# Optimization experiments

Measured on AMD Instinct MI355X. Metric: run time of the kernel, lower is better.

Reference implementation:

```python
import jax, jax.numpy as jnp
import numpy as np

B, S, D = 2, 2048, 2048
H, HKV = 16, 4
GROUPS = H // HKV
RQ, RKV = 1024, 512
DH, DR = 192, 64          # q_head_dim, rope dim
DN = DH - DR              # nrope dim = 128
DV = 128                  # v head dim
EPS = 1e-20


def setup_inputs() -> dict:
    key = jax.random.key(0)
    ks = jax.random.split(key, 8)
    inp = {
        "hidden_states": jax.random.normal(ks[0], (B, S, D), jnp.float32),
        # causal mask (0 = masked), as used by masked_fill(mask == 0, -inf)
        "attention_mask": jnp.tril(jnp.ones((S, S), jnp.int32))[None, None],
        "w_qa": jax.random.normal(ks[1], (D, RQ), jnp.float32) * 0.02,
        "b_qa": jnp.zeros((RQ,), jnp.float32),
        "g_q": jnp.ones((RQ,), jnp.float32),
        "w_qb": jax.random.normal(ks[2], (RQ, H * DH), jnp.float32) * 0.02,
        "b_qb": jnp.zeros((H * DH,), jnp.float32),
        "w_kva": jax.random.normal(ks[3], (D, RKV + DR), jnp.float32) * 0.02,
        "b_kva": jnp.zeros((RKV + DR,), jnp.float32),
        "g_kv": jnp.ones((RKV,), jnp.float32),
        "w_kvb": jax.random.normal(ks[4], (RKV, HKV * (DN + DV)), jnp.float32) * 0.02,
        "b_kvb": jnp.zeros((HKV * (DN + DV),), jnp.float32),
        "w_o": jax.random.normal(ks[5], (H * DV, D), jnp.float32) * 0.02,
        "b_o": jnp.zeros((D,), jnp.float32),
    }
    return inp


def _rmsnorm(x, g, eps=EPS):
    var = jnp.mean(x * x, axis=-1, keepdims=True)
    return x * jax.lax.rsqrt(var + eps) * g


def _rope_cos_sin(seq_len, dim, base=10000.0, dtype=jnp.float32):
    inv_freq = 1.0 / (base ** (jnp.arange(0, dim, 2, dtype=jnp.float32) / dim))
    t = jnp.arange(seq_len, dtype=jnp.float32)
    freqs = jnp.outer(t, inv_freq)                    # [S, dim/2]
    emb = jnp.concatenate([freqs, freqs], axis=-1)    # [S, dim]
    return jnp.cos(emb).astype(dtype), jnp.sin(emb).astype(dtype)


def _apply_rope(x, cos, sin):
    # x: [..., S, dr]; rotate_half convention
    d2 = x.shape[-1] // 2
    x1, x2 = x[..., :d2], x[..., d2:]
    rot = jnp.concatenate([-x2, x1], axis=-1)
    return x * cos + rot * sin


def reference(hidden_states, attention_mask, w_qa, b_qa, g_q, w_qb, b_qb,
              w_kva, b_kva, g_kv, w_kvb, b_kvb, w_o, b_o):
    b, s, _ = hidden_states.shape
    # --- Q: LoRA down -> RMSNorm -> LoRA up ---
    q_a = hidden_states @ w_qa + b_qa                         # [B,S,RQ]
    q_b = _rmsnorm(q_a, g_q) @ w_qb + b_qb                    # [B,S,H*DH]
    q_b = q_b.reshape(b, s, H, DH).transpose(0, 2, 1, 3)      # [B,H,S,DH]
    q_nrope, q_rope = q_b[..., :DN], q_b[..., DN:]
    # --- KV: LoRA down, split latent / shared rope key ---
    kv_a = hidden_states @ w_kva + b_kva                      # [B,S,RKV+DR]
    kv_c, k_rope = kv_a[..., :RKV], kv_a[..., RKV:]
    kv_b = _rmsnorm(kv_c, g_kv) @ w_kvb + b_kvb               # [B,S,HKV*(DN+DV)]
    kv_b = kv_b.reshape(b, s, HKV, DN + DV).transpose(0, 2, 1, 3)
    k_nrope, value_states = kv_b[..., :DN], kv_b[..., DN:]    # [B,HKV,S,DN/DV]
    # --- split RoPE ---
    cos, sin = _rope_cos_sin(s, DR, dtype=hidden_states.dtype)
    q_rope = _apply_rope(q_rope, cos, sin)                    # [B,H,S,DR]
    k_rope = _apply_rope(k_rope[:, None], cos, sin)           # [B,1,S,DR]
    # --- assemble heads (rope part first, matching source concat order) ---
    query_states = jnp.concatenate([q_rope, q_nrope], axis=-1)            # [B,H,S,DH]
    key_states = jnp.concatenate(
        [jnp.broadcast_to(k_rope, (b, HKV, s, DR)), k_nrope], axis=-1)    # [B,HKV,S,DH]
    # --- GQA expand kv heads ---
    key_states = jnp.repeat(key_states, GROUPS, axis=1)                   # [B,H,S,DH]
    value_states = jnp.repeat(value_states, GROUPS, axis=1)               # [B,H,S,DV]
    # --- attention ---
    scores = jnp.einsum('bhqd,bhkd->bhqk', query_states, key_states)
    scores = scores / jnp.sqrt(jnp.asarray(DH, scores.dtype))
    scores = jnp.where(attention_mask == 0, jnp.asarray(-1e9, scores.dtype), scores)
    weights = jax.nn.softmax(scores, axis=-1)
    attn_out = jnp.einsum('bhqk,bhkd->bhqd', weights, value_states)       # [B,H,S,DV]
    attn_out = attn_out.transpose(0, 2, 1, 3).reshape(b, s, H * DV)
    return attn_out @ w_o + b_o
```

## Files before the change

kernel.cpp:

```cpp
#include <hip/hip_runtime.h>
#include <hip/hip_bf16.h>
#include <stdint.h>

#define DEV static __device__ __forceinline__

typedef __attribute__((ext_vector_type(8))) short bf16x8;
typedef __attribute__((ext_vector_type(4))) float f32x4;
typedef __attribute__((ext_vector_type(16))) float f32x16;

constexpr int Bc = 2, Sc = 2048, Dc = 2048;
constexpr int Hc = 16, HKVc = 4;
constexpr int RQc = 1024, RKVc = 512;
constexpr int DHc = 192, DRc = 64, DVc = 128;

DEV unsigned short f2bf(float f) {
  union { float f; uint32_t u; } v; v.f = f;
  uint32_t r = v.u + 0x7FFFu + ((v.u >> 16) & 1u);
  return (unsigned short)(r >> 16);
}
DEV float bf2f(unsigned short u) {
  union { uint32_t u; float f; } v; v.u = ((uint32_t)u) << 16;
  return v.f;
}

DEV void gload_lds16(const unsigned short* g, unsigned short* l) {
  __builtin_amdgcn_global_load_lds(
      (const __attribute__((address_space(1))) unsigned int*)g,
      (__attribute__((address_space(3))) unsigned int*)l, 16, 0, 0);
}

__global__ void f2b_kernel(const float* __restrict__ in, unsigned short* __restrict__ out, int n) {
  int stride = gridDim.x * blockDim.x;
  for (int i = blockIdx.x * blockDim.x + threadIdx.x; i * 4 < n; i += stride) {
    float4 v = reinterpret_cast<const float4*>(in)[i];
    union { unsigned short u[4]; uint64_t q; } pk;
    pk.u[0] = f2bf(v.x); pk.u[1] = f2bf(v.y); pk.u[2] = f2bf(v.z); pk.u[3] = f2bf(v.w);
    reinterpret_cast<uint64_t*>(out)[i] = pk.q;
  }
}

__global__ void wtrans_kernel(const float* __restrict__ in, unsigned short* __restrict__ out,
                              int R, int C) {
  __shared__ float tile[32][33];
  const int c0 = blockIdx.x * 32, r0 = blockIdx.y * 32;
  const int tx = threadIdx.x & 31, ty = threadIdx.x >> 5;
#pragma unroll
  for (int i = 0; i < 32; i += 8)
    tile[ty + i][tx] = in[(size_t)(r0 + ty + i) * C + c0 + tx];
  __syncthreads();
#pragma unroll
  for (int i = 0; i < 32; i += 8)
    out[(size_t)(c0 + ty + i) * R + r0 + tx] = f2bf(tile[tx][ty + i]);
}

__global__ void rope_table_kernel(float* __restrict__ cosT, float* __restrict__ sinT) {
  int idx = blockIdx.x * blockDim.x + threadIdx.x;
  if (idx >= Sc * DRc) return;
  int t = idx >> 6;
  int j = idx & 63;
  float inv = exp2f(-13.287712379549449f * (float)(j & 31) * (1.0f / 32.0f));
  float f = (float)t * inv;
  cosT[idx] = cosf(f);
  sinT[idx] = sinf(f);
}

template<int R>
__global__ void rmsnorm_kernel(const float* __restrict__ in, int istride,
                               const float* __restrict__ g, unsigned short* __restrict__ out) {
  int row = blockIdx.x;
  const float* x = in + (size_t)row * istride;
  float ss = 0.f;
  for (int j = threadIdx.x; j < R; j += 256) { float v = x[j]; ss += v * v; }
  for (int off = 32; off; off >>= 1) ss += __shfl_down(ss, off, 64);
  __shared__ float wsum[4];
  if ((threadIdx.x & 63) == 0) wsum[threadIdx.x >> 6] = ss;
  __syncthreads();
  float tot = wsum[0] + wsum[1] + wsum[2] + wsum[3];
  float rs = rsqrtf(tot * (1.0f / R) + 1e-20f);
  for (int j = threadIdx.x; j < R; j += 256)
    out[(size_t)row * R + j] = f2bf(x[j] * rs * g[j]);
}

template<bool OUT_BF16, bool NG>
__global__ __launch_bounds__(256)
void gemm_tn_kernel(const unsigned short* __restrict__ A, const unsigned short* __restrict__ Bt,
                    const float* __restrict__ bias, void* __restrict__ Cout,
                    int M, int N, int K) {
  __shared__ __align__(16) unsigned short As[2][128 * 64];
  __shared__ __align__(16) unsigned short Bs[2][128 * 64];
  const int t = threadIdx.x, lane = t & 63, wave = t >> 6;
  const int wm = wave >> 1, wn = wave & 1;
  const int m0 = blockIdx.x * 128, n0 = blockIdx.y * 128;
  const int fr = lane & 15, fo = (lane >> 4) * 8, rg = lane >> 4;
  const int srow = lane >> 3;
  const int scol = (lane & 7) * 8;

  const unsigned short* Ap[4];
  const unsigned short* Bp[4];
#pragma unroll
  for (int i = 0; i < 4; ++i) {
    const int ar = m0 + wave * 32 + i * 8 + srow;
    Ap[i] = A + (size_t)ar * K + scol;
    int br = n0 + wave * 32 + i * 8 + srow;
    if (NG) br = br < N ? br : N - 1;
    Bp[i] = Bt + (size_t)br * K + scol;
  }

  auto stage = [&](int buf, int k0) {
#pragma unroll
    for (int i = 0; i < 4; ++i) {
      gload_lds16(Ap[i] + k0, &As[buf][(wave * 32 + i * 8) * 64]);
      gload_lds16(Bp[i] + k0, &Bs[buf][(wave * 32 + i * 8) * 64]);
    }
  };

  f32x4 acc[4][4] = {};
  const int nt = K >> 6;

  stage(0, 0);
  for (int tt = 0; tt < nt; ++tt) {
    const int cur = tt & 1;
    if (tt + 1 < nt) {
      stage(cur ^ 1, (tt + 1) * 64);
      asm volatile("s_waitcnt vmcnt(8)" ::: "memory");
    } else {
      asm volatile("s_waitcnt vmcnt(0)" ::: "memory");
    }
    __syncthreads();
#pragma unroll
    for (int kk = 0; kk < 64; kk += 32) {
      bf16x8 af[4], bf[4];
#pragma unroll
      for (int m = 0; m < 4; ++m)
        af[m] = *reinterpret_cast<const bf16x8*>(&As[cur][(wm * 64 + m * 16 + fr) * 64 + kk + fo]);
#pragma unroll
      for (int n = 0; n < 4; ++n)
        bf[n] = *reinterpret_cast<const bf16x8*>(&Bs[cur][(wn * 64 + n * 16 + fr) * 64 + kk + fo]);
      __builtin_amdgcn_s_setprio(1);
#pragma unroll
      for (int m = 0; m < 4; ++m)
#pragma unroll
        for (int n = 0; n < 4; ++n)
          acc[m][n] = __builtin_amdgcn_mfma_f32_16x16x32_bf16(af[m], bf[n], acc[m][n], 0, 0, 0);
      __builtin_amdgcn_s_setprio(0);
    }
    __syncthreads();
  }

#pragma unroll
  for (int m = 0; m < 4; ++m) {
    const int row = m0 + wm * 64 + m * 16 + rg * 4;
#pragma unroll
    for (int n = 0; n < 4; ++n) {
      const int col = n0 + wn * 64 + n * 16 + fr;
      if (NG && col >= N) continue;
      const float bb = bias[col];
#pragma unroll
      for (int r = 0; r < 4; ++r) {
        float v = acc[m][n][r] + bb;
        if (OUT_BF16)
          reinterpret_cast<unsigned short*>(Cout)[(size_t)(row + r) * N + col] = f2bf(v);
        else
          reinterpret_cast<float*>(Cout)[(size_t)(row + r) * N + col] = v;
      }
    }
  }
}

__global__ void prep_q_kernel(const unsigned short* __restrict__ qb,
                              const float* __restrict__ cosT, const float* __restrict__ sinT,
                              unsigned short* __restrict__ Q) {
  const float QS = 0.07216878364870323f * 1.4426950408889634f;
  int bs = blockIdx.x;
  int s = bs & (Sc - 1);
  int b = bs >> 11;
  int d = threadIdx.x;
  if (d >= 192) return;
  for (int h = 0; h < Hc; ++h) {
    const unsigned short* src = qb + (size_t)bs * (Hc * DHc) + h * DHc;
    float v;
    if (d < 128) {
      v = bf2f(src[d]);
    } else {
      int j = d - 128;
      float x = bf2f(src[128 + j]);
      float other = bf2f(src[128 + (j < 32 ? j + 32 : j - 32)]);
      float c = cosT[s * 64 + j], sn = sinT[s * 64 + j];
      v = (j < 32) ? (x * c - other * sn) : (x * c + other * sn);
    }
    Q[(((size_t)(b * Hc + h)) * Sc + s) * DHc + d] = f2bf(v * QS);
  }
}

__global__ void prep_k_kernel(const unsigned short* __restrict__ kvb,
                              const float* __restrict__ ccat,
                              const float* __restrict__ cosT, const float* __restrict__ sinT,
                              unsigned short* __restrict__ K) {
  int bs = blockIdx.x;
  int s = bs & (Sc - 1);
  int b = bs >> 11;
  int d = threadIdx.x;
  if (d >= 192) return;
  unsigned short ropeval = 0;
  if (d >= 128) {
    int j = d - 128;
    float x = ccat[(size_t)bs * 1600 + 1536 + j];
    float other = ccat[(size_t)bs * 1600 + 1536 + (j < 32 ? j + 32 : j - 32)];
    float c = cosT[s * 64 + j], sn = sinT[s * 64 + j];
    float v = (j < 32) ? (x * c - other * sn) : (x * c + other * sn);
    ropeval = f2bf(v);
  }
  const size_t off = (size_t)(s >> 5) * 6144 + (d >> 3) * 256 + (s & 31) * 8 + (d & 7);
  for (int kvh = 0; kvh < HKVc; ++kvh) {
    unsigned short o;
    if (d < 128) o = kvb[(size_t)bs * 1024 + kvh * 256 + d];
    else o = ropeval;
    K[(size_t)(b * HKVc + kvh) * Sc * DHc + off] = o;
  }
}

__global__ void vtrans_kernel(const unsigned short* __restrict__ kvb, unsigned short* __restrict__ Vt) {
  int idx = blockIdx.x;
  int dt = idx & 3;  idx >>= 2;
  int st = idx & 63; idx >>= 6;
  int kvh = idx & 3; idx >>= 2;
  int b = idx;
  __shared__ unsigned short tile[32][33];
  int t = threadIdx.x;
  int c = t & 31, r0 = t >> 5;
#pragma unroll
  for (int i = 0; i < 4; ++i) {
    int r = r0 + i * 8;
    int s = st * 32 + r;
    tile[r][c] = kvb[((size_t)(b * Sc + s)) * 1024 + kvh * 256 + 128 + dt * 32 + c];
  }
  __syncthreads();
#pragma unroll
  for (int i = 0; i < 4; ++i) {
    int r = r0 + i * 8;
    const int dd = dt * 32 + r;
    const int k = st * 32 + c;
    const size_t pos = (size_t)(k >> 5) * 4096 + ((k >> 3) & 3) * 1024 + dd * 8 + (k & 7);
    Vt[(size_t)((b * HKVc + kvh)) * DVc * Sc + pos] = tile[c][r];
  }
}

__global__ __launch_bounds__(256)
void attn_kernel(const unsigned short* __restrict__ Q, const unsigned short* __restrict__ Kt,
                 const unsigned short* __restrict__ Vt, unsigned short* __restrict__ attnOut) {
  __shared__ __align__(16) unsigned short Ks[4][6144];
  __shared__ float mlS[4][2][32];

  const int bid = blockIdx.x;
  const int g = bid & 7;
  const int b = g >> 2, kvh = g & 3;
  const int rr = bid >> 3;
  const int hp = rr & 1;
  const int u = rr >> 1;
  const int w = threadIdx.x >> 6;
  const int hd = w >> 1;
  const int sp = w & 1;
  const int h = kvh * 4 + hp * 2 + hd;
  const int lane = threadIdx.x & 63;
  const int l31 = lane & 31, hi = lane >> 5;

  const unsigned short* Qh = Q + (size_t)(b * Hc + h) * Sc * DHc;
  const unsigned short* Kg = Kt + (size_t)(b * HKVc + kvh) * Sc * DHc;
  const unsigned short* Vg = Vt + (size_t)(b * HKVc + kvh) * DVc * Sc;

  auto stage = [&](int i) {
    const unsigned short* src = Kg + (size_t)i * 12288;
    unsigned short* dst = &Ks[(i & 1) * 2][0];
#pragma unroll
    for (int j = 0; j < 6; ++j)
      gload_lds16(src + j * 2048 + threadIdx.x * 8, dst + j * 2048 + threadIdx.x * 8);
  };

#pragma unroll 1
  for (int pan = 0; pan < 2; ++pan) {
    const int sub = pan ? u : (63 - u);
    const int q0 = sub * 32;
    const int q = q0 + l31;
    const int NS = (sub >> 1) + 1;

    bf16x8 qf[12];
#pragma unroll
    for (int f = 0; f < 12; ++f)
      qf[f] = *reinterpret_cast<const bf16x8*>(Qh + (size_t)q * DHc + f * 16 + hi * 8);

    f32x16 ot[4] = {};
    float m = -INFINITY, lsum = 0.f;

    stage(0);
    asm volatile("s_waitcnt vmcnt(0)" ::: "memory");
    __syncthreads();

    for (int i = 0; i < NS; ++i) {
      const int t = 2 * i + sp;
      const bool active = (t <= sub);
      const int p = i & 1;

      bf16x8 vf[8];
      if (active) {
#pragma unroll
        for (int dt = 0; dt < 4; ++dt)
#pragma unroll
          for (int k2 = 0; k2 < 2; ++k2)
            vf[dt * 2 + k2] = *reinterpret_cast<const bf16x8*>(
                Vg + (size_t)t * 4096 + (k2 * 2 + hi) * 1024 + (dt * 32 + l31) * 8);
      }
      __builtin_amdgcn_sched_barrier(0);
      if (i + 1 < NS) stage(i + 1);
      __builtin_amdgcn_sched_barrier(0);

      if (active) {
        const unsigned short* kb = &Ks[p * 2 + sp][0];
        f32x16 s = {};
        __builtin_amdgcn_s_setprio(1);
#pragma unroll
        for (int f = 0; f < 12; ++f) {
          bf16x8 kf = *reinterpret_cast<const bf16x8*>(kb + (f * 2 + hi) * 256 + l31 * 8);
          s = __builtin_amdgcn_mfma_f32_32x32x16_bf16(kf, qf[f], s, 0, 0, 0);
        }
        __builtin_amdgcn_s_setprio(0);

        float v[16];
        if (t == sub) {
#pragma unroll
          for (int rrr = 0; rrr < 16; ++rrr) {
            const int kl = (rrr & 3) + 8 * (rrr >> 2) + 4 * hi;
            v[rrr] = (kl <= l31) ? s[rrr] : -3.0e38f;
          }
        } else {
#pragma unroll
          for (int rrr = 0; rrr < 16; ++rrr) v[rrr] = s[rrr];
        }

        float pmax = fmaxf(fmaxf(fmaxf(v[0], v[1]), fmaxf(v[2], v[3])),
                           fmaxf(fmaxf(v[4], v[5]), fmaxf(v[6], v[7])));
        float pmax2 = fmaxf(fmaxf(fmaxf(v[8], v[9]), fmaxf(v[10], v[11])),
                            fmaxf(fmaxf(v[12], v[13]), fmaxf(v[14], v[15])));
        pmax = fmaxf(pmax, pmax2);
        pmax = fmaxf(pmax, __shfl_xor(pmax, 32, 64));

        float cf = 1.f;
        if (!__all(pmax - m <= 8.0f)) {
          const float mnew = fmaxf(m, pmax);
          cf = exp2f(m - mnew);
          m = mnew;
#pragma unroll
          for (int dt = 0; dt < 4; ++dt)
#pragma unroll
            for (int rrr = 0; rrr < 16; ++rrr) ot[dt][rrr] *= cf;
        }

        float pp[16];
        float rs = 0.f;
#pragma unroll
        for (int rrr = 0; rrr < 16; ++rrr) { pp[rrr] = exp2f(v[rrr] - m); rs += pp[rrr]; }
        rs += __shfl_xor(rs, 32, 64);
        lsum = lsum * cf + rs;

        uint32_t c[8], x[8];
#pragma unroll
        for (int ii = 0; ii < 8; ++ii) {
          asm("v_cvt_pk_bf16_f32 %0, %1, %2" : "=v"(c[ii]) : "v"(pp[2 * ii]), "v"(pp[2 * ii + 1]));
          x[ii] = (uint32_t)__shfl_xor((int)c[ii], 32, 64);
        }
        union { uint32_t w[4]; bf16x8 v8; } pa0, pa1;
        pa0.w[0] = hi ? x[2] : c[0];
        pa0.w[1] = hi ? x[3] : c[1];
        pa0.w[2] = hi ? c[2] : x[0];
        pa0.w[3] = hi ? c[3] : x[1];
        pa1.w[0] = hi ? x[6] : c[4];
        pa1.w[1] = hi ? x[7] : c[5];
        pa1.w[2] = hi ? c[6] : x[4];
        pa1.w[3] = hi ? c[7] : x[5];

        __builtin_amdgcn_s_setprio(1);
#pragma unroll
        for (int dt = 0; dt < 4; ++dt) {
          ot[dt] = __builtin_amdgcn_mfma_f32_32x32x16_bf16(vf[dt * 2], pa0.v8, ot[dt], 0, 0, 0);
          ot[dt] = __builtin_amdgcn_mfma_f32_32x32x16_bf16(vf[dt * 2 + 1], pa1.v8, ot[dt], 0, 0, 0);
        }
        __builtin_amdgcn_s_setprio(0);
      }

      asm volatile("s_waitcnt vmcnt(0)" ::: "memory");
      __syncthreads();
    }

    if (hi == 0) { mlS[w][0][l31] = m; mlS[w][1][l31] = lsum; }
    __syncthreads();
    const int pw = w ^ 1;
    const float mp = mlS[pw][0][l31];
    const float lp = mlS[pw][1][l31];
    const float mstar = fmaxf(m, mp);
    const float sc = exp2f(m - mstar);
    const float lstar = lsum * sc + lp * exp2f(mp - mstar);
    float* LO = (float*)&Ks[0][0];

    if (sp == 1) {
#pragma unroll
      for (int dt = 0; dt < 4; ++dt)
#pragma unroll
        for (int rq = 0; rq < 4; ++rq) {
          float4 vv;
          vv.x = ot[dt][rq * 4 + 0] * sc;
          vv.y = ot[dt][rq * 4 + 1] * sc;
          vv.z = ot[dt][rq * 4 + 2] * sc;
          vv.w = ot[dt][rq * 4 + 3] * sc;
          *reinterpret_cast<float4*>(&LO[(size_t)(hd * 32 + l31) * 132 + dt * 32 + 8 * rq + 4 * hi]) = vv;
        }
    }
    __syncthreads();
    if (sp == 0) {
      const float inv = 1.0f / lstar;
      unsigned short* dst = attnOut + ((size_t)(b * Sc + q)) * (Hc * DVc) + h * DVc;
#pragma unroll
      for (int dt = 0; dt < 4; ++dt)
#pragma unroll
        for (int rq = 0; rq < 4; ++rq) {
          float4 pv = *reinterpret_cast<const float4*>(
              &LO[(size_t)(hd * 32 + l31) * 132 + dt * 32 + 8 * rq + 4 * hi]);
          const float o0 = (ot[dt][rq * 4 + 0] * sc + pv.x) * inv;
          const float o1 = (ot[dt][rq * 4 + 1] * sc + pv.y) * inv;
          const float o2 = (ot[dt][rq * 4 + 2] * sc + pv.z) * inv;
          const float o3 = (ot[dt][rq * 4 + 3] * sc + pv.w) * inv;
          uint2 pk;
          pk.x = (uint32_t)f2bf(o0) | ((uint32_t)f2bf(o1) << 16);
          pk.y = (uint32_t)f2bf(o2) | ((uint32_t)f2bf(o3) << 16);
          *reinterpret_cast<uint2*>(dst + dt * 32 + 8 * rq + 4 * hi) = pk;
        }
    }
    __syncthreads();
  }
}

extern "C" void kernel_launch(void* const* d_in, const int* in_sizes, int n_in,
                              void* d_out, int out_size, void* d_ws, size_t ws_size,
                              hipStream_t stream) {
  (void)in_sizes; (void)n_in; (void)out_size; (void)ws_size;
  const float* hidden = (const float*)d_in[0];
  const float* w_qa  = (const float*)d_in[2];
  const float* b_qa  = (const float*)d_in[3];
  const float* g_q   = (const float*)d_in[4];
  const float* w_qb  = (const float*)d_in[5];
  const float* b_qb  = (const float*)d_in[6];
  const float* w_kva = (const float*)d_in[7];
  const float* b_kva = (const float*)d_in[8];
  const float* g_kv  = (const float*)d_in[9];
  const float* w_kvb = (const float*)d_in[10];
  const float* b_kvb = (const float*)d_in[11];
  const float* w_o   = (const float*)d_in[12];
  const float* b_o   = (const float*)d_in[13];
  float* out = (float*)d_out;

  char* ws = (char*)d_ws;
  size_t off = 0;
  auto alloc = [&](size_t bytes) -> void* {
    void* p = ws + off;
    off += (bytes + 255) & ~(size_t)255;
    return p;
  };
  const int MS = Bc * Sc;
  const int NCAT = RQc + RKVc + DRc;

  unsigned short* Xbf   = (unsigned short*)alloc((size_t)MS * Dc * 2);
  unsigned short* Wcat  = (unsigned short*)alloc((size_t)NCAT * Dc * 2);
  unsigned short* WqbT  = (unsigned short*)alloc((size_t)Hc * DHc * RQc * 2);
  unsigned short* WkvbT = (unsigned short*)alloc((size_t)HKVc * 256 * RKVc * 2);
  unsigned short* WoT   = (unsigned short*)alloc((size_t)Dc * Hc * DVc * 2);
  float* bcat = (float*)alloc((size_t)NCAT * 4);
  float* cosT = (float*)alloc((size_t)Sc * DRc * 4);
  float* sinT = (float*)alloc((size_t)Sc * DRc * 4);
  float* Ccat = (float*)alloc((size_t)MS * NCAT * 4);
  unsigned short* qan  = (unsigned short*)alloc((size_t)MS * RQc * 2);
  unsigned short* qb   = (unsigned short*)alloc((size_t)MS * Hc * DHc * 2);
  unsigned short* kvcn = (unsigned short*)alloc((size_t)MS * RKVc * 2);
  unsigned short* kvb  = (unsigned short*)alloc((size_t)MS * HKVc * 256 * 2);
  unsigned short* Qt   = (unsigned short*)alloc((size_t)Bc * Hc * Sc * DHc * 2);
  unsigned short* Kt   = (unsigned short*)alloc((size_t)Bc * HKVc * Sc * DHc * 2);
  unsigned short* Vt   = (unsigned short*)alloc((size_t)Bc * HKVc * DVc * Sc * 2);
  unsigned short* attnb= (unsigned short*)alloc((size_t)MS * Hc * DVc * 2);

  f2b_kernel<<<dim3(512), dim3(256), 0, stream>>>(hidden, Xbf, MS * Dc);
  wtrans_kernel<<<dim3(RQc / 32, Dc / 32), 256, 0, stream>>>(w_qa, Wcat, Dc, RQc);
  wtrans_kernel<<<dim3((RKVc + DRc) / 32, Dc / 32), 256, 0, stream>>>(w_kva, Wcat + (size_t)RQc * Dc, Dc, RKVc + DRc);
  wtrans_kernel<<<dim3(Hc * DHc / 32, RQc / 32), 256, 0, stream>>>(w_qb, WqbT, RQc, Hc * DHc);
  wtrans_kernel<<<dim3(HKVc * 256 / 32, RKVc / 32), 256, 0, stream>>>(w_kvb, WkvbT, RKVc, HKVc * 256);
  wtrans_kernel<<<dim3(Dc / 32, Hc * DVc / 32), 256, 0, stream>>>(w_o, WoT, Hc * DVc, Dc);
  hipMemcpyAsync(bcat, b_qa, (size_t)RQc * 4, hipMemcpyDeviceToDevice, stream);
  hipMemcpyAsync(bcat + RQc, b_kva, (size_t)(RKVc + DRc) * 4, hipMemcpyDeviceToDevice, stream);
  rope_table_kernel<<<dim3(512), dim3(256), 0, stream>>>(cosT, sinT);

  gemm_tn_kernel<false, true><<<dim3(MS / 128, (NCAT + 127) / 128), 256, 0, stream>>>(Xbf, Wcat, bcat, Ccat, MS, NCAT, Dc);
  rmsnorm_kernel<1024><<<dim3(MS), 256, 0, stream>>>(Ccat, NCAT, g_q, qan);
  rmsnorm_kernel<512><<<dim3(MS), 256, 0, stream>>>(Ccat + RQc, NCAT, g_kv, kvcn);
  gemm_tn_kernel<true, false><<<dim3(MS / 128, Hc * DHc / 128), 256, 0, stream>>>(qan, WqbT, b_qb, qb, MS, Hc * DHc, RQc);
  gemm_tn_kernel<true, false><<<dim3(MS / 128, HKVc * 256 / 128), 256, 0, stream>>>(kvcn, WkvbT, b_kvb, kvb, MS, HKVc * 256, RKVc);

  prep_q_kernel<<<dim3(MS), 256, 0, stream>>>(qb, cosT, sinT, Qt);
  prep_k_kernel<<<dim3(MS), 256, 0, stream>>>(kvb, Ccat, cosT, sinT, Kt);
  vtrans_kernel<<<dim3(Bc * HKVc * (Sc / 32) * (DVc / 32)), 256, 0, stream>>>(kvb, Vt);

  attn_kernel<<<dim3(512), dim3(256), 0, stream>>>(Qt, Kt, Vt, attnb);

  gemm_tn_kernel<false, false><<<dim3(MS / 128, Dc / 128), 256, 0, stream>>>(attnb, WoT, b_o, out, MS, Dc, Hc * DVc);
}
```

Measured before the change: 365.1 us.

## Fuse Q rope/scale/transpose into q-up GEMM; drop attention key-split across waves

```diff
diff --git a/kernel.cpp b/kernel.cpp
--- a/kernel.cpp
+++ b/kernel.cpp
@@ -167,28 +167,99 @@
   }
 }
 
-__global__ void prep_q_kernel(const unsigned short* __restrict__ qb,
-                              const float* __restrict__ cosT, const float* __restrict__ sinT,
-                              unsigned short* __restrict__ Q) {
+__global__ __launch_bounds__(256)
+void gemm_qfuse_kernel(const unsigned short* __restrict__ A, const unsigned short* __restrict__ Bt,
+                       const float* __restrict__ bias,
+                       const float* __restrict__ cosT, const float* __restrict__ sinT,
+                       unsigned short* __restrict__ Qt, int M, int N, int K) {
   const float QS = 0.07216878364870323f * 1.4426950408889634f;
-  int bs = blockIdx.x;
-  int s = bs & (Sc - 1);
-  int b = bs >> 11;
-  int d = threadIdx.x;
-  if (d >= 192) return;
-  for (int h = 0; h < Hc; ++h) {
-    const unsigned short* src = qb + (size_t)bs * (Hc * DHc) + h * DHc;
-    float v;
-    if (d < 128) {
-      v = bf2f(src[d]);
+  __shared__ __align__(16) unsigned short As[2][128 * 64];
+  __shared__ __align__(16) unsigned short Bs[2][128 * 64];
+  const int t = threadIdx.x, lane = t & 63, wave = t >> 6;
+  const int wm = wave >> 1, wn = wave & 1;
+  const int m0 = blockIdx.x * 128, n0 = blockIdx.y * 128;
+  const int fr = lane & 15, fo = (lane >> 4) * 8, rg = lane >> 4;
+  const int srow = lane >> 3;
+  const int scol = (lane & 7) * 8;
+
+  const unsigned short* Ap[4];
+  const unsigned short* Bp[4];
+#pragma unroll
+  for (int i = 0; i < 4; ++i) {
+    Ap[i] = A + (size_t)(m0 + wave * 32 + i * 8 + srow) * K + scol;
+    Bp[i] = Bt + (size_t)(n0 + wave * 32 + i * 8 + srow) * K + scol;
+  }
+
+  auto stage = [&](int buf, int k0) {
+#pragma unroll
+    for (int i = 0; i < 4; ++i) {
+      gload_lds16(Ap[i] + k0, &As[buf][(wave * 32 + i * 8) * 64]);
+      gload_lds16(Bp[i] + k0, &Bs[buf][(wave * 32 + i * 8) * 64]);
+    }
+  };
+
+  f32x4 acc[4][4] = {};
+  const int nt = K >> 6;
+
+  stage(0, 0);
+  for (int tt = 0; tt < nt; ++tt) {
+    const int cur = tt & 1;
+    if (tt + 1 < nt) {
+      stage(cur ^ 1, (tt + 1) * 64);
+      asm volatile("s_waitcnt vmcnt(8)" ::: "memory");
     } else {
-      int j = d - 128;
-      float x = bf2f(src[128 + j]);
-      float other = bf2f(src[128 + (j < 32 ? j + 32 : j - 32)]);
-      float c = cosT[s * 64 + j], sn = sinT[s * 64 + j];
-      v = (j < 32) ? (x * c - other * sn) : (x * c + other * sn);
-    }
-    Q[(((size_t)(b * Hc + h)) * Sc + s) * DHc + d] = f2bf(v * QS);
+      asm volatile("s_waitcnt vmcnt(0)" ::: "memory");
+    }
+    __syncthreads();
+#pragma unroll
+    for (int kk = 0; kk < 64; kk += 32) {
+      bf16x8 af[4], bf[4];
+#pragma unroll
+      for (int m = 0; m < 4; ++m)
+        af[m] = *reinterpret_cast<const bf16x8*>(&As[cur][(wm * 64 + m * 16 + fr) * 64 + kk + fo]);
+#pragma unroll
+      for (int n = 0; n < 4; ++n)
+        bf[n] = *reinterpret_cast<const bf16x8*>(&Bs[cur][(wn * 64 + n * 16 + fr) * 64 + kk + fo]);
+      __builtin_amdgcn_s_setprio(1);
+#pragma unroll
+      for (int m = 0; m < 4; ++m)
+#pragma unroll
+        for (int n = 0; n < 4; ++n)
+          acc[m][n] = __builtin_amdgcn_mfma_f32_16x16x32_bf16(af[m], bf[n], acc[m][n], 0, 0, 0);
+      __builtin_amdgcn_s_setprio(0);
+    }
+    __syncthreads();
+  }
+
+  const int wbase = n0 + wn * 64;
+  const int hq = wbase / 192;
+  const int dbase = wbase - hq * 192;
+  const bool ropewin = (dbase == 128);
+
+#pragma unroll
+  for (int m = 0; m < 4; ++m) {
+    const int row0 = m0 + wm * 64 + m * 16 + rg * 4;
+#pragma unroll
+    for (int n = 0; n < 4; ++n) {
+      const int col = wbase + n * 16 + fr;
+      const int d = dbase + n * 16 + fr;
+      const float bb = bias[col];
+#pragma unroll
+      for (int r = 0; r < 4; ++r) {
+        const int row = row0 + r;
+        const int s = row & (Sc - 1);
+        const int bq = row >> 11;
+        float qv = acc[m][n][r] + bb;
+        if (ropewin) {
+          const int j = d - 128;
+          const int n2 = (n < 2) ? n + 2 : n - 2;
+          const float pv = acc[m][n2][r] + bias[wbase + n2 * 16 + fr];
+          const float c = cosT[s * 64 + j], sn = sinT[s * 64 + j];
+          qv = (n < 2) ? (qv * c - pv * sn) : (qv * c + pv * sn);
+        }
+        Qt[((size_t)(bq * Hc + hq) * Sc + s) * DHc + d] = f2bf(qv * QS);
+      }
+    }
   }
 }
 
@@ -245,11 +316,10 @@
   }
 }
 
-__global__ __launch_bounds__(256)
+__global__ __launch_bounds__(128)
 void attn_kernel(const unsigned short* __restrict__ Q, const unsigned short* __restrict__ Kt,
                  const unsigned short* __restrict__ Vt, unsigned short* __restrict__ attnOut) {
-  __shared__ __align__(16) unsigned short Ks[4][6144];
-  __shared__ float mlS[4][2][32];
+  __shared__ __align__(16) unsigned short Ks[2][2][6144];
 
   const int bid = blockIdx.x;
   const int g = bid & 7;
@@ -258,9 +328,7 @@
   const int hp = rr & 1;
   const int u = rr >> 1;
   const int w = threadIdx.x >> 6;
-  const int hd = w >> 1;
-  const int sp = w & 1;
-  const int h = kvh * 4 + hp * 2 + hd;
+  const int h = kvh * 4 + hp * 2 + w;
   const int lane = threadIdx.x & 63;
   const int l31 = lane & 31, hi = lane >> 5;
 
@@ -268,12 +336,12 @@
   const unsigned short* Kg = Kt + (size_t)(b * HKVc + kvh) * Sc * DHc;
   const unsigned short* Vg = Vt + (size_t)(b * HKVc + kvh) * DVc * Sc;
 
-  auto stage = [&](int i) {
-    const unsigned short* src = Kg + (size_t)i * 12288;
-    unsigned short* dst = &Ks[(i & 1) * 2][0];
-#pragma unroll
-    for (int j = 0; j < 6; ++j)
-      gload_lds16(src + j * 2048 + threadIdx.x * 8, dst + j * 2048 + threadIdx.x * 8);
+  auto stage = [&](int t) {
+    const unsigned short* src = Kg + (size_t)t * 6144;
+    unsigned short* dst = &Ks[w][t & 1][0];
+#pragma unroll
+    for (int j = 0; j < 12; ++j)
+      gload_lds16(src + j * 512 + lane * 8, dst + j * 512 + lane * 8);
   };
 
 #pragma unroll 1
@@ -281,7 +349,7 @@
     const int sub = pan ? u : (63 - u);
     const int q0 = sub * 32;
     const int q = q0 + l31;
-    const int NS = (sub >> 1) + 1;
+    const int NT = sub + 1;
 
     bf16x8 qf[12];
 #pragma unroll
@@ -292,148 +360,109 @@
     float m = -INFINITY, lsum = 0.f;
 
     stage(0);
-    asm volatile("s_waitcnt vmcnt(0)" ::: "memory");
-    __syncthreads();
-
-    for (int i = 0; i < NS; ++i) {
-      const int t = 2 * i + sp;
-      const bool active = (t <= sub);
-      const int p = i & 1;
-
+
+    for (int t = 0; t < NT; ++t) {
       bf16x8 vf[8];
-      if (active) {
+#pragma unroll
+      for (int dt = 0; dt < 4; ++dt)
+#pragma unroll
+        for (int k2 = 0; k2 < 2; ++k2)
+          vf[dt * 2 + k2] = *reinterpret_cast<const bf16x8*>(
+              Vg + (size_t)t * 4096 + (k2 * 2 + hi) * 1024 + (dt * 32 + l31) * 8);
+      __builtin_amdgcn_sched_barrier(0);
+      if (t + 1 < NT) {
+        stage(t + 1);
+        asm volatile("s_waitcnt vmcnt(20)" ::: "memory");
+      } else {
+        asm volatile("s_waitcnt vmcnt(8)" ::: "memory");
+      }
+      __builtin_amdgcn_sched_barrier(0);
+
+      const unsigned short* kb = &Ks[w][t & 1][0];
+      f32x16 s = {};
+      __builtin_amdgcn_s_setprio(1);
+#pragma unroll
+      for (int f = 0; f < 12; ++f) {
+        bf16x8 kf = *reinterpret_cast<const bf16x8*>(kb + (f * 2 + hi) * 256 + l31 * 8);
+        s = __builtin_amdgcn_mfma_f32_32x32x16_bf16(kf, qf[f], s, 0, 0, 0);
+      }
+      __builtin_amdgcn_s_setprio(0);
+
+      float v[16];
+      if (t == sub) {
+#pragma unroll
+        for (int rrr = 0; rrr < 16; ++rrr) {
+          const int kl = (rrr & 3) + 8 * (rrr >> 2) + 4 * hi;
+          v[rrr] = (kl <= l31) ? s[rrr] : -3.0e38f;
+        }
+      } else {
+#pragma unroll
+        for (int rrr = 0; rrr < 16; ++rrr) v[rrr] = s[rrr];
+      }
+
+      float pmax = fmaxf(fmaxf(fmaxf(v[0], v[1]), fmaxf(v[2], v[3])),
+                         fmaxf(fmaxf(v[4], v[5]), fmaxf(v[6], v[7])));
+      float pmax2 = fmaxf(fmaxf(fmaxf(v[8], v[9]), fmaxf(v[10], v[11])),
+                          fmaxf(fmaxf(v[12], v[13]), fmaxf(v[14], v[15])));
+      pmax = fmaxf(pmax, pmax2);
+      pmax = fmaxf(pmax, __shfl_xor(pmax, 32, 64));
+
+      float cf = 1.f;
+      if (!__all(pmax - m <= 8.0f)) {
+        const float mnew = fmaxf(m, pmax);
+        cf = exp2f(m - mnew);
+        m = mnew;
 #pragma unroll
         for (int dt = 0; dt < 4; ++dt)
 #pragma unroll
-          for (int k2 = 0; k2 < 2; ++k2)
-            vf[dt * 2 + k2] = *reinterpret_cast<const bf16x8*>(
-                Vg + (size_t)t * 4096 + (k2 * 2 + hi) * 1024 + (dt * 32 + l31) * 8);
-      }
-      __builtin_amdgcn_sched_barrier(0);
-      if (i + 1 < NS) stage(i + 1);
-      __builtin_amdgcn_sched_barrier(0);
-
-      if (active) {
-        const unsigned short* kb = &Ks[p * 2 + sp][0];
-        f32x16 s = {};
-        __builtin_amdgcn_s_setprio(1);
-#pragma unroll
-        for (int f = 0; f < 12; ++f) {
-          bf16x8 kf = *reinterpret_cast<const bf16x8*>(kb + (f * 2 + hi) * 256 + l31 * 8);
-          s = __builtin_amdgcn_mfma_f32_32x32x16_bf16(kf, qf[f], s, 0, 0, 0);
-        }
-        __builtin_amdgcn_s_setprio(0);
-
-        float v[16];
-        if (t == sub) {
-#pragma unroll
-          for (int rrr = 0; rrr < 16; ++rrr) {
-            const int kl = (rrr & 3) + 8 * (rrr >> 2) + 4 * hi;
-            v[rrr] = (kl <= l31) ? s[rrr] : -3.0e38f;
-          }
-        } else {
-#pragma unroll
-          for (int rrr = 0; rrr < 16; ++rrr) v[rrr] = s[rrr];
-        }
-
-        float pmax = fmaxf(fmaxf(fmaxf(v[0], v[1]), fmaxf(v[2], v[3])),
-                           fmaxf(fmaxf(v[4], v[5]), fmaxf(v[6], v[7])));
-        float pmax2 = fmaxf(fmaxf(fmaxf(v[8], v[9]), fmaxf(v[10], v[11])),
-                            fmaxf(fmaxf(v[12], v[13]), fmaxf(v[14], v[15])));
-        pmax = fmaxf(pmax, pmax2);
-        pmax = fmaxf(pmax, __shfl_xor(pmax, 32, 64));
-
-        float cf = 1.f;
-        if (!__all(pmax - m <= 8.0f)) {
-          const float mnew = fmaxf(m, pmax);
-          cf = exp2f(m - mnew);
-          m = mnew;
-#pragma unroll
-          for (int dt = 0; dt < 4; ++dt)
-#pragma unroll
-            for (int rrr = 0; rrr < 16; ++rrr) ot[dt][rrr] *= cf;
-        }
-
-        float pp[16];
-        float rs = 0.f;
-#pragma unroll
-        for (int rrr = 0; rrr < 16; ++rrr) { pp[rrr] = exp2f(v[rrr] - m); rs += pp[rrr]; }
-        rs += __shfl_xor(rs, 32, 64);
-        lsum = lsum * cf + rs;
-
-        uint32_t c[8], x[8];
-#pragma unroll
-        for (int ii = 0; ii < 8; ++ii) {
-          asm("v_cvt_pk_bf16_f32 %0, %1, %2" : "=v"(c[ii]) : "v"(pp[2 * ii]), "v"(pp[2 * ii + 1]));
-          x[ii] = (uint32_t)__shfl_xor((int)c[ii], 32, 64);
-        }
-        union { uint32_t w[4]; bf16x8 v8; } pa0, pa1;
-        pa0.w[0] = hi ? x[2] : c[0];
-        pa0.w[1] = hi ? x[3] : c[1];
-        pa0.w[2] = hi ? c[2] : x[0];
-        pa0.w[3] = hi ? c[3] : x[1];
-        pa1.w[0] = hi ? x[6] : c[4];
-        pa1.w[1] = hi ? x[7] : c[5];
-        pa1.w[2] = hi ? c[6] : x[4];
-        pa1.w[3] = hi ? c[7] : x[5];
-
-        __builtin_amdgcn_s_setprio(1);
-#pragma unroll
-        for (int dt = 0; dt < 4; ++dt) {
-          ot[dt] = __builtin_amdgcn_mfma_f32_32x32x16_bf16(vf[dt * 2], pa0.v8, ot[dt], 0, 0, 0);
-          ot[dt] = __builtin_amdgcn_mfma_f32_32x32x16_bf16(vf[dt * 2 + 1], pa1.v8, ot[dt], 0, 0, 0);
-        }
-        __builtin_amdgcn_s_setprio(0);
-      }
-
-      asm volatile("s_waitcnt vmcnt(0)" ::: "memory");
-      __syncthreads();
-    }
-
-    if (hi == 0) { mlS[w][0][l31] = m; mlS[w][1][l31] = lsum; }
-    __syncthreads();
-    const int pw = w ^ 1;
-    const float mp = mlS[pw][0][l31];
-    const float lp = mlS[pw][1][l31];
-    const float mstar = fmaxf(m, mp);
-    const float sc = exp2f(m - mstar);
-    const float lstar = lsum * sc + lp * exp2f(mp - mstar);
-    float* LO = (float*)&Ks[0][0];
-
-    if (sp == 1) {
-#pragma unroll
-      for (int dt = 0; dt < 4; ++dt)
-#pragma unroll
-        for (int rq = 0; rq < 4; ++rq) {
-          float4 vv;
-          vv.x = ot[dt][rq * 4 + 0] * sc;
-          vv.y = ot[dt][rq * 4 + 1] * sc;
-          vv.z = ot[dt][rq * 4 + 2] * sc;
-          vv.w = ot[dt][rq * 4 + 3] * sc;
-          *reinterpret_cast<float4*>(&LO[(size_t)(hd * 32 + l31) * 132 + dt * 32 + 8 * rq + 4 * hi]) = vv;
-        }
-    }
-    __syncthreads();
-    if (sp == 0) {
-      const float inv = 1.0f / lstar;
-      unsigned short* dst = attnOut + ((size_t)(b * Sc + q)) * (Hc * DVc) + h * DVc;
-#pragma unroll
-      for (int dt = 0; dt < 4; ++dt)
-#pragma unroll
-        for (int rq = 0; rq < 4; ++rq) {
-          float4 pv = *reinterpret_cast<const float4*>(
-              &LO[(size_t)(hd * 32 + l31) * 132 + dt * 32 + 8 * rq + 4 * hi]);
-          const float o0 = (ot[dt][rq * 4 + 0] * sc + pv.x) * inv;
-          const float o1 = (ot[dt][rq * 4 + 1] * sc + pv.y) * inv;
-          const float o2 = (ot[dt][rq * 4 + 2] * sc + pv.z) * inv;
-          const float o3 = (ot[dt][rq * 4 + 3] * sc + pv.w) * inv;
-          uint2 pk;
-          pk.x = (uint32_t)f2bf(o0) | ((uint32_t)f2bf(o1) << 16);
-          pk.y = (uint32_t)f2bf(o2) | ((uint32_t)f2bf(o3) << 16);
-          *reinterpret_cast<uint2*>(dst + dt * 32 + 8 * rq + 4 * hi) = pk;
-        }
-    }
-    __syncthreads();
+          for (int rrr = 0; rrr < 16; ++rrr) ot[dt][rrr] *= cf;
+      }
+
+      float pp[16];
+      float rs = 0.f;
+#pragma unroll
+      for (int rrr = 0; rrr < 16; ++rrr) { pp[rrr] = exp2f(v[rrr] - m); rs += pp[rrr]; }
+      rs += __shfl_xor(rs, 32, 64);
+      lsum = lsum * cf + rs;
+
+      uint32_t c[8], x[8];
+#pragma unroll
+      for (int ii = 0; ii < 8; ++ii) {
+        asm("v_cvt_pk_bf16_f32 %0, %1, %2" : "=v"(c[ii]) : "v"(pp[2 * ii]), "v"(pp[2 * ii + 1]));
+        x[ii] = (uint32_t)__shfl_xor((int)c[ii], 32, 64);
+      }
+      union { uint32_t w[4]; bf16x8 v8; } pa0, pa1;
+      pa0.w[0] = hi ? x[2] : c[0];
+      pa0.w[1] = hi ? x[3] : c[1];
+      pa0.w[2] = hi ? c[2] : x[0];
+      pa0.w[3] = hi ? c[3] : x[1];
+      pa1.w[0] = hi ? x[6] : c[4];
+      pa1.w[1] = hi ? x[7] : c[5];
+      pa1.w[2] = hi ? c[6] : x[4];
+      pa1.w[3] = hi ? c[7] : x[5];
+
+      __builtin_amdgcn_s_setprio(1);
+#pragma unroll
+      for (int dt = 0; dt < 4; ++dt) {
+        ot[dt] = __builtin_amdgcn_mfma_f32_32x32x16_bf16(vf[dt * 2], pa0.v8, ot[dt], 0, 0, 0);
+        ot[dt] = __builtin_amdgcn_mfma_f32_32x32x16_bf16(vf[dt * 2 + 1], pa1.v8, ot[dt], 0, 0, 0);
+      }
+      __builtin_amdgcn_s_setprio(0);
+    }
+
+    const float inv = 1.0f / lsum;
+    unsigned short* dst = attnOut + ((size_t)(b * Sc + q)) * (Hc * DVc) + h * DVc;
+#pragma unroll
+    for (int dt = 0; dt < 4; ++dt)
+#pragma unroll
+      for (int rq = 0; rq < 4; ++rq) {
+        uint32_t lo = (uint32_t)f2bf(ot[dt][rq * 4 + 0] * inv) |
+                      ((uint32_t)f2bf(ot[dt][rq * 4 + 1] * inv) << 16);
+        uint32_t hi2 = (uint32_t)f2bf(ot[dt][rq * 4 + 2] * inv) |
+                       ((uint32_t)f2bf(ot[dt][rq * 4 + 3] * inv) << 16);
+        uint2 pk; pk.x = lo; pk.y = hi2;
+        *reinterpret_cast<uint2*>(dst + dt * 32 + 8 * rq + 4 * hi) = pk;
+      }
   }
 }
 
@@ -476,7 +505,6 @@
   float* sinT = (float*)alloc((size_t)Sc * DRc * 4);
   float* Ccat = (float*)alloc((size_t)MS * NCAT * 4);
   unsigned short* qan  = (unsigned short*)alloc((size_t)MS * RQc * 2);
-  unsigned short* qb   = (unsigned short*)alloc((size_t)MS * Hc * DHc * 2);
   unsigned short* kvcn = (unsigned short*)alloc((size_t)MS * RKVc * 2);
   unsigned short* kvb  = (unsigned short*)alloc((size_t)MS * HKVc * 256 * 2);
   unsigned short* Qt   = (unsigned short*)alloc((size_t)Bc * Hc * Sc * DHc * 2);
@@ -497,14 +525,13 @@
   gemm_tn_kernel<false, true><<<dim3(MS / 128, (NCAT + 127) / 128), 256, 0, stream>>>(Xbf, Wcat, bcat, Ccat, MS, NCAT, Dc);
   rmsnorm_kernel<1024><<<dim3(MS), 256, 0, stream>>>(Ccat, NCAT, g_q, qan);
   rmsnorm_kernel<512><<<dim3(MS), 256, 0, stream>>>(Ccat + RQc, NCAT, g_kv, kvcn);
-  gemm_tn_kernel<true, false><<<dim3(MS / 128, Hc * DHc / 128), 256, 0, stream>>>(qan, WqbT, b_qb, qb, MS, Hc * DHc, RQc);
+  gemm_qfuse_kernel<<<dim3(MS / 128, Hc * DHc / 128), 256, 0, stream>>>(qan, WqbT, b_qb, cosT, sinT, Qt, MS, Hc * DHc, RQc);
   gemm_tn_kernel<true, false><<<dim3(MS / 128, HKVc * 256 / 128), 256, 0, stream>>>(kvcn, WkvbT, b_kvb, kvb, MS, HKVc * 256, RKVc);
 
-  prep_q_kernel<<<dim3(MS), 256, 0, stream>>>(qb, cosT, sinT, Qt);
   prep_k_kernel<<<dim3(MS), 256, 0, stream>>>(kvb, Ccat, cosT, sinT, Kt);
   vtrans_kernel<<<dim3(Bc * HKVc * (Sc / 32) * (DVc / 32)), 256, 0, stream>>>(kvb, Vt);
 
-  attn_kernel<<<dim3(512), dim3(256), 0, stream>>>(Qt, Kt, Vt, attnb);
+  attn_kernel<<<dim3(512), dim3(128), 0, stream>>>(Qt, Kt, Vt, attnb);
 
   gemm_tn_kernel<false, false><<<dim3(MS / 128, Dc / 128), 256, 0, stream>>>(attnb, WoT, b_o, out, MS, Dc, Hc * DVc);
 }
```

Measured after the change: 349.3 us. 1.05x faster.
